# Kernel tuning notes

Hardware: AMD Instinct MI355X
Metric: run time of the kernel (lower is better)

## Reference

```python
import jax, jax.numpy as jnp
import numpy as np

B, T, H, W, P = 2, 4, 224, 224, 16
D, DI, NS, RK, KC = 768, 1536, 16, 48, 4
DEPTH = 16
NV, NA = 196, 24                 # video/audio patches per frame
NTOT = (NV + 2 + NA + 2) * T     # 896 tokens (cls + patches + global, both modalities)
LVIS = NTOT // 2                 # 448 visible tokens


def setup_inputs():
    key = jax.random.key(0)
    ks = iter(jax.random.split(key, 64))
    def nrm(shape, s=0.02):
        return jax.random.normal(next(ks), shape, jnp.float32) * s
    inp = {}
    inp['x_v'] = jax.random.normal(next(ks), (B, 3, T, H, W), jnp.float32)
    inp['x_a'] = jax.random.normal(next(ks), (B, 64, 96 * T), jnp.float32)
    inp['patch_v_w'] = nrm((D, 3, P, P)); inp['patch_v_b'] = jnp.zeros((D,), jnp.float32)
    inp['patch_a_w'] = nrm((D, 1, P, P)); inp['patch_a_b'] = jnp.zeros((D,), jnp.float32)
    inp['pos_v'] = nrm((1, NV, D)); inp['pos_a'] = nrm((1, NA, D))
    inp['tpos_v'] = nrm((1, T, D)); inp['tpos_a'] = nrm((1, T, D))
    inp['cls_v'] = nrm((1, 1, D)); inp['cls_a'] = nrm((1, 1, D))
    inp['glob_v'] = nrm((1, 1, D)); inp['glob_a'] = nrm((1, 1, D))
    inp['norm_w'] = jnp.ones((DEPTH, D), jnp.float32)
    inp['in_w'] = nrm((DEPTH, 2 * DI, D))
    inp['conv_w'] = nrm((DEPTH, DI, KC), 0.2); inp['conv_b'] = jnp.zeros((DEPTH, DI), jnp.float32)
    inp['conv_w_b'] = nrm((DEPTH, DI, KC), 0.2); inp['conv_b_b'] = jnp.zeros((DEPTH, DI), jnp.float32)
    inp['xproj_w'] = nrm((DEPTH, RK + 2 * NS, DI))
    inp['xproj_w_b'] = nrm((DEPTH, RK + 2 * NS, DI))
    inp['dt_w'] = nrm((DEPTH, DI, RK), 0.1)
    inp['dt_w_b'] = nrm((DEPTH, DI, RK), 0.1)
    # mamba dt-bias init: inverse-softplus of dt ~ logU[1e-3, 0.1]
    lo, hi = np.log(1e-3), np.log(0.1)
    u = jax.random.uniform(next(ks), (DEPTH, DI), jnp.float32)
    dt = jnp.exp(u * (hi - lo) + lo)
    inp['dt_b'] = dt + jnp.log(-jnp.expm1(-dt))
    u2 = jax.random.uniform(next(ks), (DEPTH, DI), jnp.float32)
    dt2 = jnp.exp(u2 * (hi - lo) + lo)
    inp['dt_b_b'] = dt2 + jnp.log(-jnp.expm1(-dt2))
    alog = jnp.log(jnp.arange(1, NS + 1, dtype=jnp.float32))  # S4D-real init
    inp['A_log'] = jnp.broadcast_to(alog, (DEPTH, DI, NS)) + 0.0
    inp['A_log_b'] = jnp.broadcast_to(alog, (DEPTH, DI, NS)) + 0.0
    inp['D_par'] = jnp.ones((DEPTH, DI), jnp.float32)
    inp['D_par_b'] = jnp.ones((DEPTH, DI), jnp.float32)
    inp['out_w'] = nrm((DEPTH, D, DI))
    rng = np.random.default_rng(0)
    vi = np.stack([np.sort(rng.choice(NTOT, LVIS, replace=False)) for _ in range(B)])
    inp['vis_idx'] = jnp.asarray(vi, jnp.int32)
    return inp


def _causal_conv1d(x, w, b):
    # x: [B,L,DI]; depthwise causal conv, kernel KC
    xt = x.transpose(0, 2, 1)
    y = jax.lax.conv_general_dilated(xt, w[:, None, :], (1,), [(KC - 1, 0)], feature_group_count=DI)
    return (y + b[None, :, None]).transpose(0, 2, 1)


def _ssd(xc, dt, Bm, Cm, A, Dp):
    # selective scan: xc,dt [B,L,DI]; Bm,Cm [B,L,NS]; A [DI,NS]
    dA = jnp.exp(dt[..., None] * A)                         # B,L,DI,NS
    dBx = dt[..., None] * Bm[:, :, None, :] * xc[..., None]
    def step(h, s):
        a, bx, c = s
        h = a * h + bx
        return h, jnp.einsum('bdn,bn->bd', h, c)
    h0 = jnp.zeros((xc.shape[0], DI, NS), xc.dtype)
    _, ys = jax.lax.scan(step, h0, (jnp.swapaxes(dA, 0, 1), jnp.swapaxes(dBx, 0, 1), jnp.swapaxes(Cm, 0, 1)))
    return jnp.swapaxes(ys, 0, 1) + xc * Dp


def _mamba_dir(xi, zi, cw, cb, xw, dw, db, alog, dp):
    xc = jax.nn.silu(_causal_conv1d(xi, cw, cb))
    proj = jnp.einsum('bld,ed->ble', xc, xw)
    dtr, Bm, Cm = jnp.split(proj, [RK, RK + NS], axis=-1)
    dt = jax.nn.softplus(jnp.einsum('blr,dr->bld', dtr, dw) + db)
    y = _ssd(xc, dt, Bm, Cm, -jnp.exp(alog), dp)
    return y * jax.nn.silu(zi)


def reference(x_v, x_a, patch_v_w, patch_v_b, patch_a_w, patch_a_b, pos_v, pos_a, tpos_v, tpos_a,
              cls_v, cls_a, glob_v, glob_a, norm_w, in_w, conv_w, conv_b, conv_w_b, conv_b_b,
              xproj_w, xproj_w_b, dt_w, dt_b, dt_w_b, dt_b_b, A_log, A_log_b, D_par, D_par_b,
              out_w, vis_idx):
    Bn = x_v.shape[0]
    # video patch embed: conv3d k=(1,16,16) as unfold + matmul
    xv = x_v.transpose(0, 2, 3, 4, 1).reshape(Bn, T, H // P, P, W // P, P, 3)
    xv = xv.transpose(0, 1, 2, 4, 3, 5, 6).reshape(Bn, T, NV, P * P * 3)
    wv = patch_v_w.transpose(0, 2, 3, 1).reshape(D, -1)   # (kh,kw,c) flattening order
    xv = xv @ wv.T + patch_v_b                            # B,T,196,D
    # audio patch embed: [B,64,TA] -> [B,1,TA,64] conv2d 16x16
    TA = x_a.shape[-1]
    xa = x_a.transpose(0, 2, 1).reshape(Bn, TA // P, P, 64 // P, P)
    xa = xa.transpose(0, 1, 3, 2, 4).reshape(Bn, (TA // P) * (64 // P), P * P)
    xa = xa @ patch_a_w.reshape(D, -1).T + patch_a_b      # B, T*24, D
    xa = xa.reshape(Bn, T, NA, D)
    # spatial + temporal positional embeddings
    xv = xv + pos_v[None] + tpos_v[:, :, None, :]
    xa = xa + pos_a[None] + tpos_a[:, :, None, :]
    def add_tokens(x, cls, glob):
        BT = x.shape[0]
        return jnp.concatenate([jnp.broadcast_to(cls, (BT, 1, D)), x, jnp.broadcast_to(glob, (BT, 1, D))], 1)
    xv = add_tokens(xv.reshape(Bn * T, NV, D), cls_v, glob_v).reshape(Bn, T, NV + 2, D)
    xa = add_tokens(xa.reshape(Bn * T, NA, D), cls_a, glob_a).reshape(Bn, T, NA + 2, D)
    x = jnp.concatenate([xv, xa], 2).reshape(Bn, -1, D)   # B, 896, D
    x_vis = jnp.take_along_axis(x, vis_idx[:, :, None], axis=1)  # B, 448, D (x[~mask])

    def layer(carry, p):
        h, res = carry
        nw, iw, cw, cb, cwb, cbb, xw, xwb, dw, db, dwb, dbb, al, alb, dp, dpb, ow = p
        res = h + res                                     # fused add (drop_path=identity at eval)
        hn = res * jax.lax.rsqrt(jnp.mean(res * res, -1, keepdims=True) + 1e-5) * nw  # RMSNorm
        xz = jnp.einsum('bld,ed->ble', hn, iw)
        xi, zi = jnp.split(xz, 2, axis=-1)
        yf = _mamba_dir(xi, zi, cw, cb, xw, dw, db, al, dp)
        yb = _mamba_dir(xi[:, ::-1], zi[:, ::-1], cwb, cbb, xwb, dwb, dbb, alb, dpb)
        h = jnp.einsum('bld,ed->ble', yf + yb[:, ::-1], ow)
        return (h, res), None

    carry = (x_vis, jnp.zeros_like(x_vis))
    (h, res), _ = jax.lax.scan(layer, carry, (norm_w, in_w, conv_w, conv_b, conv_w_b, conv_b_b,
                                              xproj_w, xproj_w_b, dt_w, dt_b, dt_w_b, dt_b_b,
                                              A_log, A_log_b, D_par, D_par_b, out_w))
    # clip_return_layer=1 -> return_index=[depth-1]; only the post-loop append of the
    # final residual fires, so forward_features returns stack([residual]) of shape [1,B,L,D]
    return res[None]
```

## Files before the change

kernel.cpp:

```cpp
#include <hip/hip_runtime.h>
#include <math.h>

typedef unsigned short ushort_t;
typedef __attribute__((ext_vector_type(8))) short bf16x8;
typedef __attribute__((ext_vector_type(4))) float f32x4;
typedef __attribute__((ext_vector_type(4))) unsigned short us4;
typedef __attribute__((ext_vector_type(8))) unsigned short us8;

#define NBATCH 2
#define TT 4
#define DD 768
#define DI_ 1536
#define NS_ 16
#define RK_ 48
#define KC_ 4
#define DEPTH_ 16
#define NRUN 15
#define LV 448
#define NROWS (NBATCH*LV)
#define NCH 7
#define CLEN 64
#define WLAYER 4128768
#define WL8 (WLAYER/8)

__device__ __forceinline__ float silu_f(float x) { return x / (1.f + __expf(-x)); }
__device__ __forceinline__ ushort_t f2bf(float x) {
  unsigned int u = __float_as_uint(x);
  return (ushort_t)((u + 0x7FFFu + ((u >> 16) & 1u)) >> 16);
}
__device__ __forceinline__ float bf2f(ushort_t h) {
  return __uint_as_float(((unsigned int)h) << 16);
}

typedef const __attribute__((address_space(1))) unsigned int* gas1_t;
typedef __attribute__((address_space(3))) unsigned int* las3_t;
__device__ __forceinline__ void gll16(const ushort_t* g, ushort_t* l) {
  __builtin_amdgcn_global_load_lds((gas1_t)g, (las3_t)l, 16, 0, 0);
}

__global__ __launch_bounds__(256) void mfma_gemm(
    const ushort_t* __restrict__ A, const ushort_t* __restrict__ A2, int lda,
    const ushort_t* __restrict__ W, const ushort_t* __restrict__ W2, int ldw,
    const float* __restrict__ bias, const float* __restrict__ bias2,
    float* __restrict__ C, float* __restrict__ C2, int ldc,
    int M, int K, int nkChunks, long partStride, int epi)
{
  int z = blockIdx.z;
  int dir = z / nkChunks, chunk = z - dir * nkChunks;
  if (dir) { A = A2; W = W2; C = C2; bias = bias2; }
  int kChunk = K / nkChunks;
  int kbeg = chunk * kChunk;
  if (nkChunks > 1) C += (long)chunk * partStride;

  __shared__ __align__(16) ushort_t At[128 * 32];
  __shared__ __align__(16) ushort_t Bt[128 * 32];

  int tid = threadIdx.x, wv = tid >> 6, lane = tid & 63;
  int m0 = blockIdx.y * 128, n0 = blockIdx.x * 128;

  int S0 = wv * 128 + lane, S1 = S0 + 64;
  int r0 = S0 >> 2, g0 = (S0 & 3) ^ ((r0 >> 1) & 3);
  int r1 = S1 >> 2, g1 = (S1 & 3) ^ ((r1 >> 1) & 3);
  const ushort_t* a0 = A + (size_t)min(m0 + r0, M - 1) * lda + g0 * 8 + kbeg;
  const ushort_t* a1 = A + (size_t)min(m0 + r1, M - 1) * lda + g1 * 8 + kbeg;
  const ushort_t* b0 = W + (size_t)(n0 + r0) * ldw + g0 * 8 + kbeg;
  const ushort_t* b1 = W + (size_t)(n0 + r1) * ldw + g1 * 8 + kbeg;
  ushort_t* lA0 = At + S0 * 8; ushort_t* lA1 = At + S1 * 8;
  ushort_t* lB0 = Bt + S0 * 8; ushort_t* lB1 = Bt + S1 * 8;

  int wr = wv >> 1, wc = wv & 1;
  int rl = lane & 15, gl = lane >> 4;
  int offA[4], offB[4];
#pragma unroll
  for (int i = 0; i < 4; ++i) {
    int ra = wr * 64 + i * 16 + rl;
    offA[i] = ra * 32 + ((gl ^ ((ra >> 1) & 3)) * 8);
    int rb = wc * 64 + i * 16 + rl;
    offB[i] = rb * 32 + ((gl ^ ((rb >> 1) & 3)) * 8);
  }

  f32x4 acc[4][4] = {};
  int nk = kChunk >> 5;
  for (int t = 0; t < nk; ++t) {
    int ko = t << 5;
    gll16(a0 + ko, lA0); gll16(a1 + ko, lA1);
    gll16(b0 + ko, lB0); gll16(b1 + ko, lB1);
    __syncthreads();
    bf16x8 af[4], bw[4];
#pragma unroll
    for (int i = 0; i < 4; ++i) {
      af[i] = *(const bf16x8*)(At + offA[i]);
      bw[i] = *(const bf16x8*)(Bt + offB[i]);
    }
#pragma unroll
    for (int i = 0; i < 4; ++i)
#pragma unroll
      for (int j = 0; j < 4; ++j)
        acc[i][j] = __builtin_amdgcn_mfma_f32_16x16x32_bf16(af[i], bw[j], acc[i][j], 0, 0, 0);
    __syncthreads();
  }

#pragma unroll
  for (int i = 0; i < 4; ++i) {
    int row0 = m0 + wr * 64 + i * 16 + gl * 4;
#pragma unroll
    for (int q = 0; q < 4; ++q) {
      int row = row0 + q;
      if (row >= M) continue;
#pragma unroll
      for (int j = 0; j < 4; ++j) {
        int col = n0 + wc * 64 + j * 16 + rl;
        float v = acc[i][j][q];
        if (bias) v += bias[col];
        if (epi & 1) v = (v > 20.f) ? v : log1pf(__expf(v));
        if (epi & 2) ((ushort_t*)C)[(size_t)row * ldc + col] = f2bf(v);
        else C[(size_t)row * ldc + col] = v;
      }
    }
  }
}

__global__ __launch_bounds__(256) void cast4_k(const float* __restrict__ s, ushort_t* __restrict__ d, int n4)
{
  int i = blockIdx.x * 256 + threadIdx.x;
  if (i >= n4) return;
  f32x4 v = *(const f32x4*)(s + i * 4);
  us4 o = { f2bf(v[0]), f2bf(v[1]), f2bf(v[2]), f2bf(v[3]) };
  *(us4*)(d + i * 4) = o;
}

__global__ __launch_bounds__(256) void cast_all8_k(
    const float* __restrict__ iw0, const float* __restrict__ ow0,
    const float* __restrict__ xw0, const float* __restrict__ xwb0,
    const float* __restrict__ dw0, const float* __restrict__ dwb0,
    ushort_t* __restrict__ wall, int nl)
{
  int i = blockIdx.x * 256 + threadIdx.x;
  if (i >= nl * WL8) return;
  int l = i / WL8;
  int j = (i - l * WL8) * 8;
  const float* src = nullptr;
  int j2 = j;
  if (j2 < 2359296) src = iw0 + (size_t)l * 2359296 + j2;
  else {
    j2 -= 2359296;
    if (j2 < 1179648) src = ow0 + (size_t)l * 1179648 + j2;
    else {
      j2 -= 1179648;
      if (j2 < 393216) {
        const float* xs = xw0 + (size_t)l * 122880;
        if (j2 >= 196608) { j2 -= 196608; xs = xwb0 + (size_t)l * 122880; }
        int r = j2 / 1536, k = j2 - r * 1536;
        if (r < 80) src = xs + r * 1536 + k;
      } else {
        j2 -= 393216;
        const float* ds = dw0 + (size_t)l * 73728;
        if (j2 >= 98304) { j2 -= 98304; ds = dwb0 + (size_t)l * 73728; }
        int d = j2 >> 6, k = j2 & 63;
        if (k < 48) src = ds + d * 48 + k;
      }
    }
  }
  f32x4 v0 = {0.f, 0.f, 0.f, 0.f}, v1 = {0.f, 0.f, 0.f, 0.f};
  if (src) { v0 = *(const f32x4*)src; v1 = *(const f32x4*)(src + 4); }
  us8 o = { f2bf(v0[0]), f2bf(v0[1]), f2bf(v0[2]), f2bf(v0[3]),
            f2bf(v1[0]), f2bf(v1[1]), f2bf(v1[2]), f2bf(v1[3]) };
  *(us8*)(wall + (size_t)l * WLAYER + j) = o;
}

__global__ __launch_bounds__(256) void im2col_v(const float* __restrict__ xv, ushort_t* __restrict__ Av)
{
  int i = blockIdx.x * 256 + threadIdx.x;
  if (i >= 1568 * 768) return;
  int m = i / 768, k = i % 768;
  int c = k >> 8, r = k & 255;
  int kh = r >> 4, kw = r & 15;
  int bt = m / 196, n = m % 196;
  int b = bt / TT, t = bt % TT;
  int hb = n / 14, wb = n % 14;
  Av[i] = f2bf(xv[(size_t)b * 602112 + (size_t)c * 200704 + t * 50176 + (hb * 16 + kh) * 224 + wb * 16 + kw]);
}

__global__ __launch_bounds__(256) void im2col_a(const float* __restrict__ xa, ushort_t* __restrict__ Aa)
{
  int i = blockIdx.x * 256 + threadIdx.x;
  if (i >= 192 * 256) return;
  int m = i / 256, k = i % 256;
  int kh = k >> 4, kw = k & 15;
  int b = m / 96, q = m % 96;
  int tb = q >> 2, fb = q & 3;
  Aa[i] = f2bf(xa[(size_t)b * 24576 + (fb * 16 + kw) * 384 + tb * 16 + kh]);
}

__global__ __launch_bounds__(256) void assemble_k(
    const float* __restrict__ tokv, const float* __restrict__ toka,
    const float* __restrict__ pos_v, const float* __restrict__ pos_a,
    const float* __restrict__ tpos_v, const float* __restrict__ tpos_a,
    const float* __restrict__ cls_v, const float* __restrict__ cls_a,
    const float* __restrict__ glob_v, const float* __restrict__ glob_a,
    const int* __restrict__ vis_idx,
    float* __restrict__ h, float* __restrict__ res)
{
  int i = blockIdx.x * 256 + threadIdx.x;
  if (i >= NROWS * DD) return;
  int d = i % DD;
  int bl = i / DD;
  int r = bl % LV, b = bl / LV;
  int tok = vis_idx[b * LV + r];
  int t = tok / 224, q = tok % 224;
  float v;
  if (q == 0) v = cls_v[d];
  else if (q <= 196) {
    int n = q - 1;
    v = tokv[((size_t)(b * TT + t) * 196 + n) * DD + d] + pos_v[n * DD + d] + tpos_v[t * DD + d];
  } else if (q == 197) v = glob_v[d];
  else if (q == 198) v = cls_a[d];
  else if (q <= 222) {
    int n = q - 199;
    v = toka[((size_t)b * 96 + t * 24 + n) * DD + d] + pos_a[n * DD + d] + tpos_a[t * DD + d];
  } else v = glob_a[d];
  h[i] = v;
  res[i] = 0.f;
}

__global__ __launch_bounds__(256) void rmsnorm_k(
    const float* __restrict__ hsrc, const float* __restrict__ part,
    float* __restrict__ res, ushort_t* __restrict__ hn, const float* __restrict__ nw)
{
  int row = blockIdx.x;
  float* rp = res + (size_t)row * DD;
  ushort_t* op = hn + (size_t)row * DD;
  int tid = threadIdx.x;
  float v[3];
  float ss = 0.f;
#pragma unroll
  for (int i = 0; i < 3; ++i) {
    int c = tid + i * 256;
    float x;
    if (part) {
      x = part[(size_t)row * DD + c] + part[688128 + (size_t)row * DD + c]
        + part[2 * 688128 + (size_t)row * DD + c] + part[3 * 688128 + (size_t)row * DD + c];
    } else {
      x = hsrc[(size_t)row * DD + c];
    }
    x += rp[c];
    v[i] = x;
    ss += x * x;
  }
  for (int m = 1; m < 64; m <<= 1) ss += __shfl_xor(ss, m, 64);
  __shared__ float sred[4];
  if ((tid & 63) == 0) sred[tid >> 6] = ss;
  __syncthreads();
  float tot = sred[0] + sred[1] + sred[2] + sred[3];
  float sc = rsqrtf(tot / (float)DD + 1e-5f);
#pragma unroll
  for (int i = 0; i < 3; ++i) {
    int c = tid + i * 256;
    rp[c] = v[i];
    op[c] = f2bf(v[i] * sc * nw[c]);
  }
}

__global__ __launch_bounds__(256) void conv_k(
    const ushort_t* __restrict__ xz,
    const float* __restrict__ cw, const float* __restrict__ cb,
    const float* __restrict__ cwb, const float* __restrict__ cbb,
    ushort_t* __restrict__ xcFb, ushort_t* __restrict__ xcBb)
{
  int i = blockIdx.x * 256 + threadIdx.x;
  if (i >= NROWS * (DI_ / 4)) return;
  int dv = (i % (DI_ / 4)) * 4;
  int bl = i / (DI_ / 4);
  int l = bl % LV, b = bl / LV;
  const ushort_t* xzb = xz + (size_t)b * LV * (2 * DI_);
  f32x4 accf = *(const f32x4*)(cb + dv);
  f32x4 accb = *(const f32x4*)(cbb + dv);
  f32x4 tf[4], tb[4];
#pragma unroll
  for (int e = 0; e < 4; ++e) {
    tf[e] = *(const f32x4*)(cw + (dv + e) * 4);
    tb[e] = *(const f32x4*)(cwb + (dv + e) * 4);
  }
#pragma unroll
  for (int j = 0; j < 4; ++j) {
    int lp = l - 3 + j;
    if (lp >= 0) {
      us4 xf = *(const us4*)(xzb + (size_t)lp * (2 * DI_) + dv);
      us4 xb = *(const us4*)(xzb + (size_t)(LV - 1 - lp) * (2 * DI_) + dv);
#pragma unroll
      for (int e = 0; e < 4; ++e) {
        accf[e] += bf2f(xf[e]) * tf[e][j];
        accb[e] += bf2f(xb[e]) * tb[e][j];
      }
    }
  }
  us4 of, ob;
#pragma unroll
  for (int e = 0; e < 4; ++e) {
    of[e] = f2bf(silu_f(accf[e]));
    ob[e] = f2bf(silu_f(accb[e]));
  }
  *(us4*)(xcFb + (size_t)bl * DI_ + dv) = of;
  *(us4*)(xcBb + (size_t)bl * DI_ + dv) = ob;
}

__global__ __launch_bounds__(256) void reduce_pack_k(
    const float* __restrict__ pF, const float* __restrict__ pB,
    float* __restrict__ prF, float* __restrict__ prB,
    ushort_t* __restrict__ dF, ushort_t* __restrict__ dB)
{
  int i = blockIdx.x * 256 + threadIdx.x;
  if (i >= NROWS * 128) return;
  int dir = blockIdx.y;
  const float* part = dir ? pB : pF;
  float* proj = dir ? prB : prF;
  ushort_t* dtr = dir ? dB : dF;
  int row = i >> 7, col = i & 127;
  float s = 0.f;
  if (col < 80) {
#pragma unroll
    for (int c = 0; c < 8; ++c) s += part[c * (NROWS * 128) + i];
    proj[row * 80 + col] = s;
  }
  if (col < 64) dtr[(row << 6) + col] = f2bf(col < 48 ? s : 0.f);
}

__global__ __launch_bounds__(256) void scanA_k(
    const ushort_t* __restrict__ xcFb, const ushort_t* __restrict__ dtF, const float* __restrict__ prF,
    const ushort_t* __restrict__ xcBb, const ushort_t* __restrict__ dtB, const float* __restrict__ prB,
    const float* __restrict__ AlF, const float* __restrict__ AlB,
    float* __restrict__ hloc, float* __restrict__ Pb)
{
  int dir = blockIdx.z;
  const ushort_t* xc = dir ? xcBb : xcFb;
  const ushort_t* dt = dir ? dtB : dtF;
  const float* pr = dir ? prB : prF;
  const float* Al = dir ? AlB : AlF;
  int c = blockIdx.y;
  int g = blockIdx.x * 16 + (threadIdx.x >> 4);
  int n = threadIdx.x & 15;
  int b = g / DI_, d = g % DI_;
  float An = -__expf(Al[d * NS_ + n]);
  const ushort_t* xcp = xc + (size_t)b * LV * DI_ + d;
  const ushort_t* dtp = dt + (size_t)b * LV * DI_ + d;
  const float* prp = pr + (size_t)b * LV * 80;
  int l0 = c * CLEN;
  float hs = 0.f, S = 0.f;
  float dtv = bf2f(dtp[(size_t)l0 * DI_]);
  float xcv = bf2f(xcp[(size_t)l0 * DI_]);
  float bn  = prp[l0 * 80 + 48 + n];
  for (int kk = 0; kk < CLEN; ++kk) {
    float dtv_n = 0.f, xcv_n = 0.f, bn_n = 0.f;
    if (kk < CLEN - 1) {
      int l1 = l0 + kk + 1;
      dtv_n = bf2f(dtp[(size_t)l1 * DI_]);
      xcv_n = bf2f(xcp[(size_t)l1 * DI_]);
      bn_n  = prp[l1 * 80 + 48 + n];
    }
    hs = __expf(dtv * An) * hs + dtv * bn * xcv;
    S += dtv;
    dtv = dtv_n; xcv = xcv_n; bn = bn_n;
  }
  int idx = ((dir * 3072 + g) * 6 + c) * NS_ + n;
  hloc[idx] = hs;
  Pb[idx] = __expf(An * S);
}

__global__ __launch_bounds__(256) void scanBC_k(
    const ushort_t* __restrict__ xcFb, const ushort_t* __restrict__ dtF, const float* __restrict__ prF,
    const ushort_t* __restrict__ xcBb, const ushort_t* __restrict__ dtB, const float* __restrict__ prB,
    const float* __restrict__ AlF, const float* __restrict__ AlB,
    const float* __restrict__ DpF, const float* __restrict__ DpB,
    const float* __restrict__ hloc, const float* __restrict__ Pb,
    const ushort_t* __restrict__ xz, ushort_t* __restrict__ yc)
{
  int c = blockIdx.y;
  int tid = threadIdx.x;
  int n = tid & 15, gi = (tid >> 4) & 7, dir = tid >> 7;
  int g = blockIdx.x * 8 + gi;
  int b = g / DI_, d = g % DI_;
  __shared__ float sbuf[2][8][65];

  const ushort_t* xc = dir ? xcBb : xcFb;
  const ushort_t* dt = dir ? dtB : dtF;
  const float* pr = dir ? prB : prF;
  const float* Al = dir ? AlB : AlF;
  const float* Dpp = dir ? DpB : DpF;
  int myc = dir ? (6 - c) : c;
  float An = -__expf(Al[d * NS_ + n]);
  float Dpd = Dpp[d];
  float hs = 0.f;
  for (int j = 0; j < myc; ++j) {
    int idx = ((dir * 3072 + g) * 6 + j) * NS_ + n;
    hs = Pb[idx] * hs + hloc[idx];
  }
  const ushort_t* xcp = xc + (size_t)b * LV * DI_ + d;
  const ushort_t* dtp = dt + (size_t)b * LV * DI_ + d;
  const float* prp = pr + (size_t)b * LV * 80;
  int l0 = myc * CLEN;
  float dtv = bf2f(dtp[(size_t)l0 * DI_]);
  float xcv = bf2f(xcp[(size_t)l0 * DI_]);
  float bn  = prp[l0 * 80 + 48 + n];
  float cn  = prp[l0 * 80 + 64 + n];
  for (int kk = 0; kk < CLEN; ++kk) {
    float dtv_n = 0.f, xcv_n = 0.f, bn_n = 0.f, cn_n = 0.f;
    if (kk < CLEN - 1) {
      int l1 = l0 + kk + 1;
      dtv_n = bf2f(dtp[(size_t)l1 * DI_]);
      xcv_n = bf2f(xcp[(size_t)l1 * DI_]);
      bn_n  = prp[l1 * 80 + 48 + n];
      cn_n  = prp[l1 * 80 + 64 + n];
    }
    hs = __expf(dtv * An) * hs + dtv * bn * xcv;
    float p = hs * cn;
    p += __shfl_xor(p, 1, 16);
    p += __shfl_xor(p, 2, 16);
    p += __shfl_xor(p, 4, 16);
    p += __shfl_xor(p, 8, 16);
    if (n == 0) {
      int off = dir ? (CLEN - 1 - kk) : kk;
      sbuf[dir][gi][off] = p + xcv * Dpd;
    }
    dtv = dtv_n; xcv = xcv_n; bn = bn_n; cn = cn_n;
  }
  __syncthreads();
  for (int oid = tid; oid < 512; oid += 256) {
    int gi2 = oid & 7, kk = oid >> 3;
    int g2 = blockIdx.x * 8 + gi2;
    int b2 = g2 / DI_, d2 = g2 % DI_;
    int l = c * CLEN + kk;
    float z = bf2f(xz[((size_t)b2 * LV + l) * 3072 + 1536 + d2]);
    float v = (sbuf[0][gi2][kk] + sbuf[1][gi2][kk]) * silu_f(z);
    yc[((size_t)b2 * LV + l) * DI_ + d2] = f2bf(v);
  }
}

__global__ __launch_bounds__(256) void final_k(
    const float* __restrict__ res, const float* __restrict__ part, float* __restrict__ out)
{
  int i = blockIdx.x * 256 + threadIdx.x;
  if (i >= NROWS * DD) return;
  out[i] = res[i] + part[i] + part[688128 + i] + part[2 * 688128 + i] + part[3 * 688128 + i];
}

extern "C" void kernel_launch(void* const* d_in, const int* in_sizes, int n_in,
                              void* d_out, int out_size, void* d_ws, size_t ws_size,
                              hipStream_t stream)
{
  const float* x_v = (const float*)d_in[0];
  const float* x_a = (const float*)d_in[1];
  const float* patch_v_w = (const float*)d_in[2];
  const float* patch_v_b = (const float*)d_in[3];
  const float* patch_a_w = (const float*)d_in[4];
  const float* patch_a_b = (const float*)d_in[5];
  const float* pos_v = (const float*)d_in[6];
  const float* pos_a = (const float*)d_in[7];
  const float* tpos_v = (const float*)d_in[8];
  const float* tpos_a = (const float*)d_in[9];
  const float* cls_v = (const float*)d_in[10];
  const float* cls_a = (const float*)d_in[11];
  const float* glob_v = (const float*)d_in[12];
  const float* glob_a = (const float*)d_in[13];
  const float* norm_w = (const float*)d_in[14];
  const float* in_w = (const float*)d_in[15];
  const float* conv_w = (const float*)d_in[16];
  const float* conv_b = (const float*)d_in[17];
  const float* conv_w_b = (const float*)d_in[18];
  const float* conv_b_b = (const float*)d_in[19];
  const float* xproj_w = (const float*)d_in[20];
  const float* xproj_w_b = (const float*)d_in[21];
  const float *dt_w, *dt_bias, *dt_w_b, *dt_bias_b;
  if (in_sizes[23] == DEPTH_ * DI_ * RK_) {
    dt_w = (const float*)d_in[22]; dt_w_b = (const float*)d_in[23];
    dt_bias = (const float*)d_in[24]; dt_bias_b = (const float*)d_in[25];
  } else {
    dt_w = (const float*)d_in[22]; dt_bias = (const float*)d_in[23];
    dt_w_b = (const float*)d_in[24]; dt_bias_b = (const float*)d_in[25];
  }
  const float* A_log = (const float*)d_in[26];
  const float* A_log_b = (const float*)d_in[27];
  const float* D_par = (const float*)d_in[28];
  const float* D_par_b = (const float*)d_in[29];
  const float* out_w = (const float*)d_in[30];
  const int* vis_idx = (const int*)d_in[31];

  float* ws = (float*)d_ws;
  float* res   = ws;
  float* hbuf  = ws + 688128;
  float* R1    = ws + 1376256;
  float* R2f   = ws + 4128768;
  float* R3    = ws + 4816896;
  float* xz    = ws + 7569408;
  float* dtFf  = ws + 10321920;
  float* dtBf  = ws + 11698176;
  float* projF = ws + 13074432;
  float* projB = ws + 13146112;
  float* wPvf  = ws + 13217792;
  float* WALLf = ws + 13512704;

  float* partF = R1;
  float* partB = R1 + 917504;
  float* hloc  = R1;
  float* Pb    = R1 + 589824;
  float* partO = R1;
  float* tokv  = R1;
  float* toka  = R1 + 1204224;
  ushort_t* Av_bf = (ushort_t*)xz;
  ushort_t* wPv   = (ushort_t*)wPvf;
  ushort_t* wPa   = (ushort_t*)dtFf;
  ushort_t* Aa_bf = ((ushort_t*)dtFf) + 196608;
  ushort_t* hn_bf = (ushort_t*)R2f;
  ushort_t* dtrF  = (ushort_t*)R2f;
  ushort_t* dtrB  = ((ushort_t*)R2f) + 57344;
  ushort_t* ycb   = (ushort_t*)R2f;
  ushort_t* xcFb = (ushort_t*)R3;
  ushort_t* xcBb = ((ushort_t*)R3) + 1376256;
  ushort_t* xzb  = (ushort_t*)xz;
  ushort_t* dtFb = (ushort_t*)dtFf;
  ushort_t* dtBb = (ushort_t*)dtBf;

  size_t need_big = ((size_t)13512704 + (size_t)NRUN * (WLAYER / 2)) * 4;
  int bigws = ws_size >= need_big;
  ushort_t* WALL = (ushort_t*)WALLf;

  dim3 blk(256);

  if (bigws)
    cast_all8_k<<<(NRUN * WL8 + 255) / 256, blk, 0, stream>>>(
        in_w, out_w, xproj_w, xproj_w_b, dt_w, dt_w_b, WALL, NRUN);

  im2col_v<<<4704, blk, 0, stream>>>(x_v, Av_bf);
  cast4_k<<<576, blk, 0, stream>>>(patch_v_w, wPv, 147456);
  cast4_k<<<192, blk, 0, stream>>>(patch_a_w, wPa, 49152);
  im2col_a<<<192, blk, 0, stream>>>(x_a, Aa_bf);
  mfma_gemm<<<dim3(6, 13, 1), blk, 0, stream>>>(Av_bf, nullptr, 768, wPv, nullptr, 768,
                                                patch_v_b, nullptr, tokv, nullptr, 768,
                                                1568, 768, 1, 0, 0);
  mfma_gemm<<<dim3(6, 2, 1), blk, 0, stream>>>(Aa_bf, nullptr, 256, wPa, nullptr, 256,
                                               patch_a_b, nullptr, toka, nullptr, 768,
                                               192, 256, 1, 0, 0);
  assemble_k<<<2688, blk, 0, stream>>>(tokv, toka, pos_v, pos_a, tpos_v, tpos_a,
                                       cls_v, cls_a, glob_v, glob_a, vis_idx, hbuf, res);

  for (int l = 0; l < NRUN; ++l) {
    const float* nw  = norm_w + l * DD;
    const float* cw  = conv_w + l * DI_ * KC_;
    const float* cb  = conv_b + l * DI_;
    const float* cwb = conv_w_b + l * DI_ * KC_;
    const float* cbb = conv_b_b + l * DI_;
    const float* dbi = dt_bias + l * DI_;
    const float* dbib = dt_bias_b + l * DI_;
    const float* al  = A_log + (size_t)l * DI_ * NS_;
    const float* alb = A_log_b + (size_t)l * DI_ * NS_;
    const float* dp  = D_par + l * DI_;
    const float* dpb = D_par_b + l * DI_;

    ushort_t* wb = bigws ? (WALL + (size_t)l * WLAYER) : WALL;
    if (!bigws)
      cast_all8_k<<<(WL8 + 255) / 256, blk, 0, stream>>>(
          in_w + (size_t)l * 2359296, out_w + (size_t)l * 1179648,
          xproj_w + (size_t)l * 122880, xproj_w_b + (size_t)l * 122880,
          dt_w + (size_t)l * 73728, dt_w_b + (size_t)l * 73728, wb, 1);
    ushort_t* wIn  = wb;
    ushort_t* wOut = wIn + 2359296;
    ushort_t* wXF  = wOut + 1179648;
    ushort_t* wXB  = wXF + 196608;
    ushort_t* wDF  = wXB + 196608;
    ushort_t* wDB  = wDF + 98304;

    rmsnorm_k<<<NROWS, blk, 0, stream>>>(hbuf, l ? partO : nullptr, res, hn_bf, nw);
    mfma_gemm<<<dim3(24, 7, 1), blk, 0, stream>>>(hn_bf, nullptr, 768, wIn, nullptr, 768,
                                                  nullptr, nullptr, (float*)xzb, nullptr, 3072,
                                                  NROWS, 768, 1, 0, 2);
    conv_k<<<1344, blk, 0, stream>>>(xzb, cw, cb, cwb, cbb, xcFb, xcBb);
    mfma_gemm<<<dim3(1, 7, 16), blk, 0, stream>>>(xcFb, xcBb, 1536, wXF, wXB, 1536,
                                                  nullptr, nullptr, partF, partB, 128,
                                                  NROWS, 1536, 8, NROWS * 128, 0);
    reduce_pack_k<<<dim3(448, 2, 1), blk, 0, stream>>>(partF, partB, projF, projB, dtrF, dtrB);
    mfma_gemm<<<dim3(12, 7, 2), blk, 0, stream>>>(dtrF, dtrB, 64, wDF, wDB, 64,
                                                  dbi, dbib, (float*)dtFb, (float*)dtBb, 1536,
                                                  NROWS, 64, 1, 0, 3);
    scanA_k<<<dim3(192, 6, 2), blk, 0, stream>>>(xcFb, dtFb, projF, xcBb, dtBb, projB,
                                                 al, alb, hloc, Pb);
    scanBC_k<<<dim3(384, NCH, 1), blk, 0, stream>>>(xcFb, dtFb, projF, xcBb, dtBb, projB,
                                                    al, alb, dp, dpb, hloc, Pb, xzb, ycb);
    mfma_gemm<<<dim3(6, 7, 4), blk, 0, stream>>>(ycb, nullptr, 1536, wOut, nullptr, 1536,
                                                 nullptr, nullptr, partO, nullptr, 768,
                                                 NROWS, 1536, 4, NROWS * DD, 0);
  }

  final_k<<<2688, blk, 0, stream>>>(res, partO, (float*)d_out);
}
```

Baseline: 2.886 ms.

## Halve GEMM M-tile, fuse dt projection into reduction, split weight casts

The MFMA GEMM tile shrinks from 128x128 to 64x128, doubling grid rows so each GEMM launches more blocks on the many-CU GPU. The separate dt-projection GEMM and the reduce/pack kernel are merged into one reddt_k kernel. It sums the x_proj partials, computes the 48-rank dt projection in fp32 from shared memory with softplus, and writes bf16 dt directly. The up-front weight cast is split into simpler per-tensor kernels and no longer casts dt weights. In exchange, each block gets less A reuse, and the dt matmul runs on scalar FMAs instead of MFMA.

```diff
diff --git a/kernel.cpp b/kernel.cpp
--- a/kernel.cpp
+++ b/kernel.cpp
@@ -20,8 +20,11 @@
 #define NROWS (NBATCH*LV)
 #define NCH 7
 #define CLEN 64
-#define WLAYER 4128768
-#define WL8 (WLAYER/8)
+
+#define WIN_SZ   (NRUN*2359296)
+#define WOUT_SZ  (NRUN*1179648)
+#define WX_SZ    (NRUN*2*196608)
+#define WALL_USH (WIN_SZ + WOUT_SZ + WX_SZ)
 
 __device__ __forceinline__ float silu_f(float x) { return x / (1.f + __expf(-x)); }
 __device__ __forceinline__ ushort_t f2bf(float x) {
@@ -52,48 +55,52 @@
   int kbeg = chunk * kChunk;
   if (nkChunks > 1) C += (long)chunk * partStride;
 
-  __shared__ __align__(16) ushort_t At[128 * 32];
+  __shared__ __align__(16) ushort_t At[64 * 32];
   __shared__ __align__(16) ushort_t Bt[128 * 32];
 
   int tid = threadIdx.x, wv = tid >> 6, lane = tid & 63;
-  int m0 = blockIdx.y * 128, n0 = blockIdx.x * 128;
-
-  int S0 = wv * 128 + lane, S1 = S0 + 64;
-  int r0 = S0 >> 2, g0 = (S0 & 3) ^ ((r0 >> 1) & 3);
-  int r1 = S1 >> 2, g1 = (S1 & 3) ^ ((r1 >> 1) & 3);
-  const ushort_t* a0 = A + (size_t)min(m0 + r0, M - 1) * lda + g0 * 8 + kbeg;
-  const ushort_t* a1 = A + (size_t)min(m0 + r1, M - 1) * lda + g1 * 8 + kbeg;
-  const ushort_t* b0 = W + (size_t)(n0 + r0) * ldw + g0 * 8 + kbeg;
-  const ushort_t* b1 = W + (size_t)(n0 + r1) * ldw + g1 * 8 + kbeg;
-  ushort_t* lA0 = At + S0 * 8; ushort_t* lA1 = At + S1 * 8;
-  ushort_t* lB0 = Bt + S0 * 8; ushort_t* lB1 = Bt + S1 * 8;
+  int m0 = blockIdx.y * 64, n0 = blockIdx.x * 128;
+
+  int rA = tid >> 2, gA = (tid & 3) ^ ((rA >> 1) & 3);
+  const ushort_t* aSrc = A + (size_t)min(m0 + rA, M - 1) * lda + gA * 8 + kbeg;
+  ushort_t* aDst = At + tid * 8;
+  int SB0 = tid, SB1 = tid + 256;
+  int rB0 = SB0 >> 2, gB0 = (SB0 & 3) ^ ((rB0 >> 1) & 3);
+  int rB1 = SB1 >> 2, gB1 = (SB1 & 3) ^ ((rB1 >> 1) & 3);
+  const ushort_t* bSrc0 = W + (size_t)(n0 + rB0) * ldw + gB0 * 8 + kbeg;
+  const ushort_t* bSrc1 = W + (size_t)(n0 + rB1) * ldw + gB1 * 8 + kbeg;
+  ushort_t* bDst0 = Bt + SB0 * 8;
+  ushort_t* bDst1 = Bt + SB1 * 8;
 
   int wr = wv >> 1, wc = wv & 1;
   int rl = lane & 15, gl = lane >> 4;
-  int offA[4], offB[4];
-#pragma unroll
-  for (int i = 0; i < 4; ++i) {
-    int ra = wr * 64 + i * 16 + rl;
+  int offA[2], offB[4];
+#pragma unroll
+  for (int i = 0; i < 2; ++i) {
+    int ra = wr * 32 + i * 16 + rl;
     offA[i] = ra * 32 + ((gl ^ ((ra >> 1) & 3)) * 8);
-    int rb = wc * 64 + i * 16 + rl;
-    offB[i] = rb * 32 + ((gl ^ ((rb >> 1) & 3)) * 8);
-  }
-
-  f32x4 acc[4][4] = {};
+  }
+#pragma unroll
+  for (int j = 0; j < 4; ++j) {
+    int rb = wc * 64 + j * 16 + rl;
+    offB[j] = rb * 32 + ((gl ^ ((rb >> 1) & 3)) * 8);
+  }
+
+  f32x4 acc[2][4] = {};
   int nk = kChunk >> 5;
   for (int t = 0; t < nk; ++t) {
     int ko = t << 5;
-    gll16(a0 + ko, lA0); gll16(a1 + ko, lA1);
-    gll16(b0 + ko, lB0); gll16(b1 + ko, lB1);
+    gll16(aSrc + ko, aDst);
+    gll16(bSrc0 + ko, bDst0);
+    gll16(bSrc1 + ko, bDst1);
     __syncthreads();
-    bf16x8 af[4], bw[4];
-#pragma unroll
-    for (int i = 0; i < 4; ++i) {
-      af[i] = *(const bf16x8*)(At + offA[i]);
-      bw[i] = *(const bf16x8*)(Bt + offB[i]);
-    }
-#pragma unroll
-    for (int i = 0; i < 4; ++i)
+    bf16x8 af[2], bw[4];
+#pragma unroll
+    for (int i = 0; i < 2; ++i) af[i] = *(const bf16x8*)(At + offA[i]);
+#pragma unroll
+    for (int j = 0; j < 4; ++j) bw[j] = *(const bf16x8*)(Bt + offB[j]);
+#pragma unroll
+    for (int i = 0; i < 2; ++i)
 #pragma unroll
       for (int j = 0; j < 4; ++j)
         acc[i][j] = __builtin_amdgcn_mfma_f32_16x16x32_bf16(af[i], bw[j], acc[i][j], 0, 0, 0);
@@ -101,8 +108,8 @@
   }
 
 #pragma unroll
-  for (int i = 0; i < 4; ++i) {
-    int row0 = m0 + wr * 64 + i * 16 + gl * 4;
+  for (int i = 0; i < 2; ++i) {
+    int row0 = m0 + wr * 32 + i * 16 + gl * 4;
 #pragma unroll
     for (int q = 0; q < 4; ++q) {
       int row = row0 + q;
@@ -129,43 +136,33 @@
   *(us4*)(d + i * 4) = o;
 }
 
-__global__ __launch_bounds__(256) void cast_all8_k(
-    const float* __restrict__ iw0, const float* __restrict__ ow0,
-    const float* __restrict__ xw0, const float* __restrict__ xwb0,
-    const float* __restrict__ dw0, const float* __restrict__ dwb0,
-    ushort_t* __restrict__ wall, int nl)
-{
-  int i = blockIdx.x * 256 + threadIdx.x;
-  if (i >= nl * WL8) return;
-  int l = i / WL8;
-  int j = (i - l * WL8) * 8;
-  const float* src = nullptr;
-  int j2 = j;
-  if (j2 < 2359296) src = iw0 + (size_t)l * 2359296 + j2;
-  else {
-    j2 -= 2359296;
-    if (j2 < 1179648) src = ow0 + (size_t)l * 1179648 + j2;
-    else {
-      j2 -= 1179648;
-      if (j2 < 393216) {
-        const float* xs = xw0 + (size_t)l * 122880;
-        if (j2 >= 196608) { j2 -= 196608; xs = xwb0 + (size_t)l * 122880; }
-        int r = j2 / 1536, k = j2 - r * 1536;
-        if (r < 80) src = xs + r * 1536 + k;
-      } else {
-        j2 -= 393216;
-        const float* ds = dw0 + (size_t)l * 73728;
-        if (j2 >= 98304) { j2 -= 98304; ds = dwb0 + (size_t)l * 73728; }
-        int d = j2 >> 6, k = j2 & 63;
-        if (k < 48) src = ds + d * 48 + k;
-      }
-    }
-  }
-  f32x4 v0 = {0.f, 0.f, 0.f, 0.f}, v1 = {0.f, 0.f, 0.f, 0.f};
-  if (src) { v0 = *(const f32x4*)src; v1 = *(const f32x4*)(src + 4); }
+__global__ __launch_bounds__(256) void cast8_k(const float* __restrict__ s, ushort_t* __restrict__ d, int n8)
+{
+  int i = blockIdx.x * 256 + threadIdx.x;
+  if (i >= n8) return;
+  f32x4 v0 = *(const f32x4*)(s + i * 8);
+  f32x4 v1 = *(const f32x4*)(s + i * 8 + 4);
   us8 o = { f2bf(v0[0]), f2bf(v0[1]), f2bf(v0[2]), f2bf(v0[3]),
             f2bf(v1[0]), f2bf(v1[1]), f2bf(v1[2]), f2bf(v1[3]) };
-  *(us8*)(wall + (size_t)l * WLAYER + j) = o;
+  *(us8*)(d + i * 8) = o;
+}
+
+__global__ __launch_bounds__(256) void castx8_k(
+    const float* __restrict__ xw0, const float* __restrict__ xwb0,
+    ushort_t* __restrict__ WX, int nl)
+{
+  int i = blockIdx.x * 256 + threadIdx.x;
+  if (i >= nl * 2 * 24576) return;
+  int ld = i / 24576;
+  int j = (i - ld * 24576) * 8;
+  int l = ld >> 1;
+  const float* xs = ((ld & 1) ? xwb0 : xw0) + (size_t)l * 122880;
+  int r = j / 1536, k = j - r * 1536;
+  f32x4 v0 = {0.f,0.f,0.f,0.f}, v1 = {0.f,0.f,0.f,0.f};
+  if (r < 80) { v0 = *(const f32x4*)(xs + r * 1536 + k); v1 = *(const f32x4*)(xs + r * 1536 + k + 4); }
+  us8 o = { f2bf(v0[0]), f2bf(v0[1]), f2bf(v0[2]), f2bf(v0[3]),
+            f2bf(v1[0]), f2bf(v1[1]), f2bf(v1[2]), f2bf(v1[3]) };
+  *(us8*)(WX + (size_t)ld * 196608 + j) = o;
 }
 
 __global__ __launch_bounds__(256) void im2col_v(const float* __restrict__ xv, ushort_t* __restrict__ Av)
@@ -304,25 +301,51 @@
   *(us4*)(xcBb + (size_t)bl * DI_ + dv) = ob;
 }
 
-__global__ __launch_bounds__(256) void reduce_pack_k(
+__global__ __launch_bounds__(256) void reddt_k(
     const float* __restrict__ pF, const float* __restrict__ pB,
     float* __restrict__ prF, float* __restrict__ prB,
-    ushort_t* __restrict__ dF, ushort_t* __restrict__ dB)
-{
-  int i = blockIdx.x * 256 + threadIdx.x;
-  if (i >= NROWS * 128) return;
+    const float* __restrict__ dwF, const float* __restrict__ dwB,
+    const float* __restrict__ dbF, const float* __restrict__ dbB,
+    ushort_t* __restrict__ dtFb, ushort_t* __restrict__ dtBb)
+{
   int dir = blockIdx.y;
   const float* part = dir ? pB : pF;
   float* proj = dir ? prB : prF;
-  ushort_t* dtr = dir ? dB : dF;
-  int row = i >> 7, col = i & 127;
-  float s = 0.f;
-  if (col < 80) {
-#pragma unroll
-    for (int c = 0; c < 8; ++c) s += part[c * (NROWS * 128) + i];
+  const float* dw = dir ? dwB : dwF;
+  const float* db = dir ? dbB : dbF;
+  ushort_t* dt = dir ? dtBb : dtFb;
+  int r0 = blockIdx.x * 8;
+  int tid = threadIdx.x;
+  __shared__ float sdtr[8][48];
+  for (int o = tid; o < 8 * 80; o += 256) {
+    int r = o / 80, col = o - (o / 80) * 80;
+    int row = r0 + r;
+    float s = 0.f;
+#pragma unroll
+    for (int c = 0; c < 8; ++c) s += part[c * (NROWS * 128) + row * 128 + col];
     proj[row * 80 + col] = s;
-  }
-  if (col < 64) dtr[(row << 6) + col] = f2bf(col < 48 ? s : 0.f);
+    if (col < 48) sdtr[r][col] = s;
+  }
+  __syncthreads();
+#pragma unroll
+  for (int q = 0; q < 6; ++q) {
+    int d = q * 256 + tid;
+    f32x4 w[12];
+#pragma unroll
+    for (int e = 0; e < 12; ++e) w[e] = *(const f32x4*)(dw + (size_t)d * 48 + e * 4);
+    float bias = db[d];
+#pragma unroll
+    for (int r = 0; r < 8; ++r) {
+      float s = bias;
+#pragma unroll
+      for (int e = 0; e < 12; ++e) {
+#pragma unroll
+        for (int u = 0; u < 4; ++u) s += sdtr[r][e * 4 + u] * w[e][u];
+      }
+      s = (s > 20.f) ? s : log1pf(__expf(s));
+      dt[(size_t)(r0 + r) * DI_ + d] = f2bf(s);
+    }
+  }
 }
 
 __global__ __launch_bounds__(256) void scanA_k(
@@ -510,8 +533,6 @@
   ushort_t* wPa   = (ushort_t*)dtFf;
   ushort_t* Aa_bf = ((ushort_t*)dtFf) + 196608;
   ushort_t* hn_bf = (ushort_t*)R2f;
-  ushort_t* dtrF  = (ushort_t*)R2f;
-  ushort_t* dtrB  = ((ushort_t*)R2f) + 57344;
   ushort_t* ycb   = (ushort_t*)R2f;
   ushort_t* xcFb = (ushort_t*)R3;
   ushort_t* xcBb = ((ushort_t*)R3) + 1376256;
@@ -519,24 +540,29 @@
   ushort_t* dtFb = (ushort_t*)dtFf;
   ushort_t* dtBb = (ushort_t*)dtBf;
 
-  size_t need_big = ((size_t)13512704 + (size_t)NRUN * (WLAYER / 2)) * 4;
+  size_t need_big = ((size_t)13512704 + (WALL_USH + 1) / 2) * 4;
   int bigws = ws_size >= need_big;
   ushort_t* WALL = (ushort_t*)WALLf;
+  ushort_t* WIN  = WALL;
+  ushort_t* WOUT = WIN + WIN_SZ;
+  ushort_t* WX   = WOUT + WOUT_SZ;
 
   dim3 blk(256);
 
-  if (bigws)
-    cast_all8_k<<<(NRUN * WL8 + 255) / 256, blk, 0, stream>>>(
-        in_w, out_w, xproj_w, xproj_w_b, dt_w, dt_w_b, WALL, NRUN);
+  if (bigws) {
+    cast8_k<<<(WIN_SZ / 8 + 255) / 256, blk, 0, stream>>>(in_w, WIN, WIN_SZ / 8);
+    cast8_k<<<(WOUT_SZ / 8 + 255) / 256, blk, 0, stream>>>(out_w, WOUT, WOUT_SZ / 8);
+    castx8_k<<<(NRUN * 2 * 24576 + 255) / 256, blk, 0, stream>>>(xproj_w, xproj_w_b, WX, NRUN);
+  }
 
   im2col_v<<<4704, blk, 0, stream>>>(x_v, Av_bf);
   cast4_k<<<576, blk, 0, stream>>>(patch_v_w, wPv, 147456);
   cast4_k<<<192, blk, 0, stream>>>(patch_a_w, wPa, 49152);
   im2col_a<<<192, blk, 0, stream>>>(x_a, Aa_bf);
-  mfma_gemm<<<dim3(6, 13, 1), blk, 0, stream>>>(Av_bf, nullptr, 768, wPv, nullptr, 768,
+  mfma_gemm<<<dim3(6, 25, 1), blk, 0, stream>>>(Av_bf, nullptr, 768, wPv, nullptr, 768,
                                                 patch_v_b, nullptr, tokv, nullptr, 768,
                                                 1568, 768, 1, 0, 0);
-  mfma_gemm<<<dim3(6, 2, 1), blk, 0, stream>>>(Aa_bf, nullptr, 256, wPa, nullptr, 256,
+  mfma_gemm<<<dim3(6, 3, 1), blk, 0, stream>>>(Aa_bf, nullptr, 256, wPa, nullptr, 256,
                                                patch_a_b, nullptr, toka, nullptr, 768,
                                                192, 256, 1, 0, 0);
   assemble_k<<<2688, blk, 0, stream>>>(tokv, toka, pos_v, pos_a, tpos_v, tpos_a,
@@ -548,6 +574,8 @@
     const float* cb  = conv_b + l * DI_;
     const float* cwb = conv_w_b + l * DI_ * KC_;
     const float* cbb = conv_b_b + l * DI_;
+    const float* dwF = dt_w + (size_t)l * DI_ * RK_;
+    const float* dwB = dt_w_b + (size_t)l * DI_ * RK_;
     const float* dbi = dt_bias + l * DI_;
     const float* dbib = dt_bias_b + l * DI_;
     const float* al  = A_log + (size_t)l * DI_ * NS_;
@@ -555,38 +583,37 @@
     const float* dp  = D_par + l * DI_;
     const float* dpb = D_par_b + l * DI_;
 
-    ushort_t* wb = bigws ? (WALL + (size_t)l * WLAYER) : WALL;
-    if (!bigws)
-      cast_all8_k<<<(WL8 + 255) / 256, blk, 0, stream>>>(
-          in_w + (size_t)l * 2359296, out_w + (size_t)l * 1179648,
-          xproj_w + (size_t)l * 122880, xproj_w_b + (size_t)l * 122880,
-          dt_w + (size_t)l * 73728, dt_w_b + (size_t)l * 73728, wb, 1);
-    ushort_t* wIn  = wb;
-    ushort_t* wOut = wIn + 2359296;
-    ushort_t* wXF  = wOut + 1179648;
-    ushort_t* wXB  = wXF + 196608;
-    ushort_t* wDF  = wXB + 196608;
-    ushort_t* wDB  = wDF + 98304;
+    ushort_t *wIn, *wOut, *wXF, *wXB;
+    if (bigws) {
+      wIn  = WIN + (size_t)l * 2359296;
+      wOut = WOUT + (size_t)l * 1179648;
+      wXF  = WX + (size_t)(l * 2) * 196608;
+      wXB  = wXF + 196608;
+    } else {
+      wIn = WALL; wOut = wIn + 2359296; wXF = wOut + 1179648; wXB = wXF + 196608;
+      cast8_k<<<(2359296 / 8 + 255) / 256, blk, 0, stream>>>(in_w + (size_t)l * 2359296, wIn, 2359296 / 8);
+      cast8_k<<<(1179648 / 8 + 255) / 256, blk, 0, stream>>>(out_w + (size_t)l * 1179648, wOut, 1179648 / 8);
+      castx8_k<<<(2 * 24576 + 255) / 256, blk, 0, stream>>>(xproj_w + (size_t)l * 122880,
+                                                            xproj_w_b + (size_t)l * 122880, wXF, 1);
+    }
 
     rmsnorm_k<<<NROWS, blk, 0, stream>>>(hbuf, l ? partO : nullptr, res, hn_bf, nw);
-    mfma_gemm<<<dim3(24, 7, 1), blk, 0, stream>>>(hn_bf, nullptr, 768, wIn, nullptr, 768,
-                                                  nullptr, nullptr, (float*)xzb, nullptr, 3072,
-                                                  NROWS, 768, 1, 0, 2);
+    mfma_gemm<<<dim3(24, 14, 1), blk, 0, stream>>>(hn_bf, nullptr, 768, wIn, nullptr, 768,
+                                                   nullptr, nullptr, (float*)xzb, nullptr, 3072,
+                                                   NROWS, 768, 1, 0, 2);
     conv_k<<<1344, blk, 0, stream>>>(xzb, cw, cb, cwb, cbb, xcFb, xcBb);
-    mfma_gemm<<<dim3(1, 7, 16), blk, 0, stream>>>(xcFb, xcBb, 1536, wXF, wXB, 1536,
-                                                  nullptr, nullptr, partF, partB, 128,
-                                                  NROWS, 1536, 8, NROWS * 128, 0);
-    reduce_pack_k<<<dim3(448, 2, 1), blk, 0, stream>>>(partF, partB, projF, projB, dtrF, dtrB);
-    mfma_gemm<<<dim3(12, 7, 2), blk, 0, stream>>>(dtrF, dtrB, 64, wDF, wDB, 64,
-                                                  dbi, dbib, (float*)dtFb, (float*)dtBb, 1536,
-                                                  NROWS, 64, 1, 0, 3);
+    mfma_gemm<<<dim3(1, 14, 16), blk, 0, stream>>>(xcFb, xcBb, 1536, wXF, wXB, 1536,
+                                                   nullptr, nullptr, partF, partB, 128,
+                                                   NROWS, 1536, 8, NROWS * 128, 0);
+    reddt_k<<<dim3(112, 2, 1), blk, 0, stream>>>(partF, partB, projF, projB,
+                                                 dwF, dwB, dbi, dbib, dtFb, dtBb);
     scanA_k<<<dim3(192, 6, 2), blk, 0, stream>>>(xcFb, dtFb, projF, xcBb, dtBb, projB,
                                                  al, alb, hloc, Pb);
     scanBC_k<<<dim3(384, NCH, 1), blk, 0, stream>>>(xcFb, dtFb, projF, xcBb, dtBb, projB,
                                                     al, alb, dp, dpb, hloc, Pb, xzb, ycb);
-    mfma_gemm<<<dim3(6, 7, 4), blk, 0, stream>>>(ycb, nullptr, 1536, wOut, nullptr, 1536,
-                                                 nullptr, nullptr, partO, nullptr, 768,
-                                                 NROWS, 1536, 4, NROWS * DD, 0);
+    mfma_gemm<<<dim3(6, 14, 4), blk, 0, stream>>>(ycb, nullptr, 1536, wOut, nullptr, 1536,
+                                                  nullptr, nullptr, partO, nullptr, 768,
+                                                  NROWS, 1536, 4, NROWS * DD, 0);
   }
 
   final_k<<<2688, blk, 0, stream>>>(res, partO, (float*)d_out);
```

Result: faster. 2.567 ms (-11.1%).
